# Performance work log

Measured on AMD Instinct MI355X. Metric: run time of the kernel, lower is better.

The kernel has to match this reference:

```python
import jax, jax.numpy as jnp
import numpy as np

B, S, H, N, NREL = 16, 2048, 1024, 128, 8


def setup_inputs() -> dict:
    key = jax.random.key(0)
    ks = jax.random.split(key, 8)
    word_emb = jax.random.normal(ks[0], (B, S, H), dtype=jnp.float32)
    num_ids = jax.random.randint(ks[1], (B, N), 0, S)  # all valid (no -1 padding)
    is_response = jax.random.randint(ks[2], (B, N), 0, 2).astype(jnp.int32)
    numbers = jax.random.normal(ks[3], (B, N), dtype=jnp.float32)
    scale = 1.0 / np.sqrt(H).astype(np.float32)
    w_alpha = jax.random.normal(ks[4], (H, 1), dtype=jnp.float32) * scale
    b_alpha = jnp.zeros((1,), dtype=jnp.float32)
    w_f = jax.random.normal(ks[5], (H, H), dtype=jnp.float32) * scale
    b_f = jnp.zeros((H,), dtype=jnp.float32)
    W_r = jax.random.normal(ks[6], (NREL, H, H), dtype=jnp.float32) * scale  # 8 bias-free relation linears
    return dict(word_emb=word_emb, num_ids=num_ids, is_response=is_response,
                numbers=numbers, w_alpha=w_alpha, b_alpha=b_alpha,
                w_f=w_f, b_f=b_f, W_r=W_r)


def reference(word_emb, num_ids, is_response, numbers, w_alpha, b_alpha, w_f, b_f, W_r):
    Bn, Sn, Hn = word_emb.shape
    Nn = num_ids.shape[1]
    mask = (num_ids >= 0)  # [B,N] valid-node mask (original uses -1 padding)
    idx = jnp.clip(num_ids, 0, Sn - 1)
    # per-batch gather: Init[b,n] = word_emb[b, num_ids[b,n]]  -> [B,N,H]
    Init = jnp.take_along_axis(word_emb, idx[:, :, None], axis=1)
    alpha = jax.nn.sigmoid(Init @ w_alpha + b_alpha)  # [B,N,1]
    # all 8 relation transforms of every sender node j: T[b,r,j,:] = Init[b,j] @ W_r[r].T
    T = jnp.einsum('bnh,rkh->brnk', Init, W_r)  # [B,8,N,H]
    # relation id r(b,i,j) = 4*(num_i>num_j) + 2*resp_i + resp_j
    gt = (numbers[:, :, None] > numbers[:, None, :]).astype(jnp.int32)  # [B,N,N]
    resp = (is_response == 1).astype(jnp.int32)
    R = 4 * gt + 2 * resp[:, :, None] + resp[:, None, :]  # [B,N,N]
    sel = jax.nn.one_hot(R, NREL, dtype=word_emb.dtype)  # [B,N,N,8]
    not_diag = ~jnp.eye(Nn, dtype=bool)
    # edge weight over sender j: alpha_j, valid i & j, i != j
    wgt = (alpha[:, None, :, 0] * mask[:, None, :] * mask[:, :, None]
           * not_diag[None]).astype(word_emb.dtype)  # [B,N,N]
    Temp = jnp.einsum('bijr,brjh->bih', sel * wgt[..., None], T)  # [B,N,H]
    n_nodes = mask.sum(axis=1)  # [B]
    denom = jnp.maximum(n_nodes - 1, 1).astype(word_emb.dtype)
    Temp = Temp / denom[:, None, None]
    out = jax.nn.relu(Init @ w_f + b_f + Temp)  # [B,N,H]
    return out
```

## Files before the change

kernel.cpp:

```cpp
#include <hip/hip_runtime.h>
#include <hip/hip_bf16.h>
#include <stdint.h>

#define B_ 16
#define S_ 2048
#define H_ 1024
#define N_ 128
#define M_ (B_*N_)
#define K5 5120
#define MP 2176

typedef __attribute__((ext_vector_type(8))) short s8vec;
typedef __attribute__((ext_vector_type(4))) short s4vec;
typedef __attribute__((ext_vector_type(4))) float f4vec;
typedef __hip_bfloat16 bf16;

__global__ void k_sortmeta(const int* __restrict__ num_ids, const int* __restrict__ is_resp,
                           const float* __restrict__ numbers,
                           int* __restrict__ sigma, int* __restrict__ newgrp,
                           int* __restrict__ respv, float* __restrict__ denom,
                           int* __restrict__ aperm, int* __restrict__ iperm,
                           int* __restrict__ meta) {
    __shared__ float nums_s[2048];
    __shared__ int sig_s[2048];
    __shared__ int s0[1024], s1[1024];
    __shared__ int cnt_s[16];
    int t = threadIdx.x;
    int g0 = 2*t, g1 = 2*t + 1;
    int b = g0 >> 7;
    int i0 = g0 & 127, i1 = g1 & 127;
    float n0 = numbers[g0], n1 = numbers[g1];
    int id0 = num_ids[g0], id1 = num_ids[g1];
    int v0 = (id0 >= 0) ? 1 : 0, v1 = (id1 >= 0) ? 1 : 0;
    int rsp0 = (is_resp[g0] == 1) ? 1 : 0, rsp1 = (is_resp[g1] == 1) ? 1 : 0;
    nums_s[g0] = n0; nums_s[g1] = n1;
    if (t < 16) cnt_s[t] = 0;
    aperm[t] = -1; aperm[t + 1024] = -1;
    if (t < MP - 2048) aperm[t + 2048] = -1;
    __syncthreads();
    const float* nb = nums_s + b*N_;
    int p0 = 0, p1 = 0;
    for (int j = 0; j < N_; ++j) {
        float nj = nb[j];
        p0 += (nj < n0 || (nj == n0 && j < i0)) ? 1 : 0;
        p1 += (nj < n1 || (nj == n1 && j < i1)) ? 1 : 0;
    }
    sig_s[b*N_ + p0] = i0;
    sig_s[b*N_ + p1] = i1;
    atomicAdd(&cnt_s[b], v0 + v1);
    __syncthreads();
    sigma[g0] = sig_s[g0]; sigma[g1] = sig_s[g1];
    {
        int cur = sig_s[g0];
        int prv = (i0 > 0) ? sig_s[g0-1] : 0;
        newgrp[g0] = (i0 == 0 || nb[cur] != nb[prv]) ? 1 : 0;
        cur = sig_s[g1];
        prv = sig_s[g1-1];
        newgrp[g1] = (nb[cur] != nb[prv]) ? 1 : 0;
    }
    respv[g0] = rsp0 | (v0 << 1);
    respv[g1] = rsp1 | (v1 << 1);
    if (t < 16) denom[t] = fmaxf((float)(cnt_s[t] - 1), 1.0f);
    int a0 = 1 - rsp0, b0 = 1 - rsp1;
    s0[t] = a0 + b0;
    s1[t] = rsp0 + rsp1;
    __syncthreads();
    for (int off = 1; off < 1024; off <<= 1) {
        int w0 = (t >= off) ? s0[t-off] : 0;
        int w1 = (t >= off) ? s1[t-off] : 0;
        __syncthreads();
        s0[t] += w0; s1[t] += w1;
        __syncthreads();
    }
    int C0 = s0[1023], C1 = s1[1023];
    int P0 = ((C0 + 127) >> 7) << 7;
    int ex0 = s0[t] - (a0 + b0);
    int ex1 = s1[t] - (rsp0 + rsp1);
    int p_a = (rsp0 == 0) ? ex0 : P0 + ex1;
    int p_b = (rsp1 == 0) ? ex0 + a0 : P0 + ex1 + rsp0;
    aperm[p_a] = g0; iperm[g0] = p_a;
    aperm[p_b] = g1; iperm[g1] = p_b;
    if (t == 0) { meta[0] = P0; meta[1] = C0; meta[2] = C1; }
}

__global__ void k_prep(const float* __restrict__ word_emb, const int* __restrict__ num_ids,
                       const float* __restrict__ w_alpha, const float* __restrict__ b_alpha,
                       const float* __restrict__ denom, const int* __restrict__ iperm,
                       const float* __restrict__ W_r, const float* __restrict__ w_f,
                       bf16* __restrict__ A, float* __restrict__ ascaled,
                       bf16* __restrict__ Wt) {
    __shared__ float lds[64][65];
    int bid = blockIdx.x;
    int t = threadIdx.x;
    if (bid < 2048) {
        int b = bid >> 7, n = bid & 127;
        int idv = num_ids[b*N_ + n];
        int valid = (idv >= 0) ? 1 : 0;
        int idx = idv < 0 ? 0 : (idv > S_-1 ? S_-1 : idv);
        int pr = iperm[b*N_ + n];
        const float4* row = (const float4*)(word_emb + ((size_t)b*S_ + idx)*H_);
        float4 v = row[t];
        float4 w = ((const float4*)w_alpha)[t];
        float part = v.x*w.x + v.y*w.y + v.z*w.z + v.w*w.w;
        union { s4vec v4; bf16 h[4]; } pk;
        pk.h[0] = __float2bfloat16(v.x);
        pk.h[1] = __float2bfloat16(v.y);
        pk.h[2] = __float2bfloat16(v.z);
        pk.h[3] = __float2bfloat16(v.w);
        *(s4vec*)(A + (size_t)pr*K5 + 4*H_ + t*4) = pk.v4;
#pragma unroll
        for (int off = 32; off > 0; off >>= 1) part += __shfl_down(part, off, 64);
        if ((t & 63) == 0) lds[0][t >> 6] = part;
        __syncthreads();
        if (t == 0) {
            float dot = lds[0][0] + lds[0][1] + lds[0][2] + lds[0][3] + b_alpha[0];
            float al = 1.0f / (1.0f + __expf(-dot));
            ascaled[b*N_ + n] = valid ? (al / denom[b]) : 0.0f;
        }
        return;
    }
    if (bid < 6144) {
        size_t o = ((size_t)(bid - 2048)*256 + t)*8;
        int cs = (int)(o >> 20);
        int c = cs >> 2, s = cs & 3;
        int r = ((s >> 1) << 2) + 2*c + (s & 1);
        size_t off = o & (size_t)(H_*H_ - 1);
        const float4* src = (const float4*)(W_r + (size_t)r*H_*H_ + off);
        float4 v0 = src[0], v1 = src[1];
        union { s8vec v8; bf16 h[8]; } pk;
        pk.h[0] = __float2bfloat16(v0.x); pk.h[1] = __float2bfloat16(v0.y);
        pk.h[2] = __float2bfloat16(v0.z); pk.h[3] = __float2bfloat16(v0.w);
        pk.h[4] = __float2bfloat16(v1.x); pk.h[5] = __float2bfloat16(v1.y);
        pk.h[6] = __float2bfloat16(v1.z); pk.h[7] = __float2bfloat16(v1.w);
        *(s8vec*)(Wt + (size_t)(c*5 + s)*H_*H_ + off) = pk.v8;
        return;
    }
    int bb = bid - 6144;
    int bi = bb & 15, bj = bb >> 4;
    int ty = t >> 4, tx = t & 15;
#pragma unroll
    for (int i = 0; i < 4; ++i) {
        int r = ty*4 + i;
        float4 v = *(const float4*)(w_f + (size_t)(bi*64 + r)*H_ + bj*64 + tx*4);
        lds[r][tx*4+0] = v.x; lds[r][tx*4+1] = v.y;
        lds[r][tx*4+2] = v.z; lds[r][tx*4+3] = v.w;
    }
    __syncthreads();
    bf16* d0 = Wt + (size_t)4*H_*H_;
    bf16* d1 = Wt + (size_t)9*H_*H_;
#pragma unroll
    for (int i = 0; i < 4; ++i) {
        int n = ty*4 + i;
        size_t doff = (size_t)(bj*64 + n)*H_ + bi*64 + tx*4;
        union { s4vec v4; bf16 h[4]; } pk;
#pragma unroll
        for (int j = 0; j < 4; ++j) pk.h[j] = __float2bfloat16(lds[tx*4+j][n]);
        *(s4vec*)(d0 + doff) = pk.v4;
        *(s4vec*)(d1 + doff) = pk.v4;
    }
}

__global__ void k_build(const float* __restrict__ ascaled, const int* __restrict__ sigma,
                        const int* __restrict__ newgrp, const int* __restrict__ respv,
                        const int* __restrict__ iperm, bf16* __restrict__ A) {
    int b = blockIdx.y;
    int h = blockIdx.x*64 + threadIdx.x;
    __shared__ float as_s[N_];
    __shared__ int sig_s[N_], ng_s[N_], rv_s[N_], pm_s[N_];
    for (int j = threadIdx.x; j < N_; j += 64) {
        as_s[j] = ascaled[b*N_ + j];
        sig_s[j] = sigma[b*N_ + j];
        ng_s[j] = newgrp[b*N_ + j];
        rv_s[j] = respv[b*N_ + j];
        pm_s[j] = iperm[b*N_ + j];
    }
    __syncthreads();
    const bf16* initcol = A + 4*H_ + h;
    float tot0 = 0.f, tot1 = 0.f;
#pragma unroll 8
    for (int i2 = 0; i2 < N_; ++i2) {
        float v = as_s[i2] * __bfloat162float(initcol[(size_t)pm_s[i2]*K5]);
        if (rv_s[i2] & 1) tot1 += v; else tot0 += v;
    }
    float cS0=0.f, cS1=0.f, cG0=0.f, cG1=0.f;
#pragma unroll 8
    for (int p = 0; p < N_; ++p) {
        int i2 = sig_s[p];
        if (ng_s[p]) { cS0 += cG0; cS1 += cG1; cG0 = 0.f; cG1 = 0.f; }
        float v = as_s[i2] * __bfloat162float(initcol[(size_t)pm_s[i2]*K5]);
        int resp = rv_s[i2] & 1;
        float vf = (rv_s[i2] >> 1) ? 1.0f : 0.0f;
        float G0 = cS0, G1 = cS1;
        float L0 = tot0 - G0 - (resp ? 0.f : v);
        float L1 = tot1 - G1 - (resp ? v : 0.f);
        bf16* Ar = A + (size_t)pm_s[i2]*K5 + h;
        Ar[0*H_] = __float2bfloat16(L0*vf);
        Ar[1*H_] = __float2bfloat16(L1*vf);
        Ar[2*H_] = __float2bfloat16(G0*vf);
        Ar[3*H_] = __float2bfloat16(G1*vf);
        if (resp) cG1 += v; else cG0 += v;
    }
}

#define BM 128
#define BN 128
#define BK 64
#define KS 4
#define KSP (K5/KS)
#define NSTEP (KSP/BK)

__global__ __launch_bounds__(256, 2) void k_gemm(const bf16* __restrict__ A,
                                                 const bf16* __restrict__ Wt,
                                                 const int* __restrict__ meta,
                                                 float* __restrict__ P) {
    __shared__ __align__(16) bf16 As0[BM*BK], As1[BM*BK];
    __shared__ __align__(16) bf16 Bs0[BN*BK], Bs1[BN*BK];
    int tid = threadIdx.x;
    int w = tid >> 6, lane = tid & 63;
    int q = lane >> 4, r = lane & 15;
    int bid = blockIdx.x;
    int wg = (bid & 7)*68 + (bid >> 3);
    int mt = wg % 17;
    int rest = wg / 17;
    int nt = rest & 7, ks = rest >> 3;
    int rowBase = mt * BM, colBase = nt * BN;
    int wm = w >> 1, wn = w & 1;
    int P0 = meta[0];
    const bf16* Wtc = Wt + ((rowBase >= P0) ? (size_t)5*H_*H_ : 0);
    const int kb = ks * KSP;

    f4vec acc[4][4];
#pragma unroll
    for (int mi = 0; mi < 4; ++mi)
#pragma unroll
        for (int ni = 0; ni < 4; ++ni)
#pragma unroll
            for (int e = 0; e < 4; ++e) acc[mi][ni][e] = 0.0f;

    auto STAGE = [&](bf16* AsB, bf16* BsB, int kin) {
        int slot = kin >> 10, koff = kin & 1023;
        const bf16* Wslot = Wtc + ((size_t)slot << 20);
#pragma unroll
        for (int j = 0; j < 4; ++j) {
            int c = tid + j*256;
            int row = c >> 3;
            int p = (c & 7) ^ (row & 7);
            const bf16* ga = A + (size_t)(rowBase + row)*K5 + kin + p*8;
            __builtin_amdgcn_global_load_lds((const __attribute__((address_space(1))) void*)ga,
                (__attribute__((address_space(3))) void*)((char*)AsB + j*4096 + w*1024), 16, 0, 0);
            const bf16* gb = Wslot + ((size_t)(colBase + row) << 10) + koff + p*8;
            __builtin_amdgcn_global_load_lds((const __attribute__((address_space(1))) void*)gb,
                (__attribute__((address_space(3))) void*)((char*)BsB + j*4096 + w*1024), 16, 0, 0);
        }
    };

    auto COMPUTE = [&](const bf16* AsB, const bf16* BsB) {
        const short* Asp = (const short*)AsB;
        const short* Bsp = (const short*)BsB;
        s8vec af[2][4], bfr[2][4];
#pragma unroll
        for (int kk = 0; kk < 2; ++kk) {
            int sl = ((kk*4 + q) ^ (r & 7)) << 3;
#pragma unroll
            for (int mi = 0; mi < 4; ++mi)
                af[kk][mi] = *(const s8vec*)(Asp + (wm*64 + mi*16 + r)*BK + sl);
#pragma unroll
            for (int ni = 0; ni < 4; ++ni)
                bfr[kk][ni] = *(const s8vec*)(Bsp + (wn*64 + ni*16 + r)*BK + sl);
        }
#pragma unroll
        for (int kk = 0; kk < 2; ++kk)
#pragma unroll
            for (int mi = 0; mi < 4; ++mi)
#pragma unroll
                for (int ni = 0; ni < 4; ++ni)
                    acc[mi][ni] = __builtin_amdgcn_mfma_f32_16x16x32_bf16(
                        af[kk][mi], bfr[kk][ni], acc[mi][ni], 0, 0, 0);
    };

    STAGE(As0, Bs0, kb);
    asm volatile("s_waitcnt vmcnt(0)" ::: "memory");
    __builtin_amdgcn_s_barrier();
    __builtin_amdgcn_sched_barrier(0);

    for (int t = 0; t < NSTEP; t += 2) {
        STAGE(As1, Bs1, kb + (t + 1)*BK);
        COMPUTE(As0, Bs0);
        asm volatile("s_waitcnt vmcnt(0)" ::: "memory");
        __builtin_amdgcn_s_barrier();
        __builtin_amdgcn_sched_barrier(0);
        if (t + 2 < NSTEP) STAGE(As0, Bs0, kb + (t + 2)*BK);
        COMPUTE(As1, Bs1);
        asm volatile("s_waitcnt vmcnt(0)" ::: "memory");
        __builtin_amdgcn_s_barrier();
        __builtin_amdgcn_sched_barrier(0);
    }

    float* Pk = P + (size_t)ks*MP*H_;
#pragma unroll
    for (int mi = 0; mi < 4; ++mi) {
#pragma unroll
        for (int ni = 0; ni < 4; ++ni) {
            int cc = colBase + wn*64 + ni*16 + r;
#pragma unroll
            for (int e = 0; e < 4; ++e) {
                int rr = rowBase + wm*64 + mi*16 + q*4 + e;
                Pk[(size_t)rr*H_ + cc] = acc[mi][ni][e];
            }
        }
    }
}

__global__ void k_epi(const float* __restrict__ P, const int* __restrict__ iperm,
                      const float* __restrict__ b_f, float* __restrict__ out) {
    int row = blockIdx.x;
    int pr = iperm[row];
    int t = threadIdx.x;
    float4 v0 = ((const float4*)(P + ((size_t)0*MP + pr)*H_))[t];
    float4 v1 = ((const float4*)(P + ((size_t)1*MP + pr)*H_))[t];
    float4 v2 = ((const float4*)(P + ((size_t)2*MP + pr)*H_))[t];
    float4 v3 = ((const float4*)(P + ((size_t)3*MP + pr)*H_))[t];
    float4 bv = ((const float4*)b_f)[t];
    float4 o;
    o.x = fmaxf(v0.x + v1.x + v2.x + v3.x + bv.x, 0.0f);
    o.y = fmaxf(v0.y + v1.y + v2.y + v3.y + bv.y, 0.0f);
    o.z = fmaxf(v0.z + v1.z + v2.z + v3.z + bv.z, 0.0f);
    o.w = fmaxf(v0.w + v1.w + v2.w + v3.w + bv.w, 0.0f);
    ((float4*)(out + (size_t)row*H_))[t] = o;
}

extern "C" void kernel_launch(void* const* d_in, const int* in_sizes, int n_in,
                              void* d_out, int out_size, void* d_ws, size_t ws_size,
                              hipStream_t stream) {
    (void)in_sizes; (void)n_in; (void)out_size; (void)ws_size;
    const float* word_emb = (const float*)d_in[0];
    const int*   num_ids  = (const int*)d_in[1];
    const int*   is_resp  = (const int*)d_in[2];
    const float* numbers  = (const float*)d_in[3];
    const float* w_alpha  = (const float*)d_in[4];
    const float* b_alpha  = (const float*)d_in[5];
    const float* w_f      = (const float*)d_in[6];
    const float* b_f      = (const float*)d_in[7];
    const float* W_r      = (const float*)d_in[8];
    float* out = (float*)d_out;

    char* ws = (char*)d_ws;
    bf16*  Aws     = (bf16*)(ws);
    bf16*  Wt      = (bf16*)(ws + 22282240);
    float* Pbuf    = (float*)(ws + 43253760);
    float* ascaled = (float*)(ws + 78905344);
    int*   sigma   = (int*)(ws + 78913536);
    int*   newgrp  = (int*)(ws + 78921728);
    int*   respv   = (int*)(ws + 78929920);
    float* denom   = (float*)(ws + 78938112);
    int*   aperm   = (int*)(ws + 78938176);
    int*   iperm   = (int*)(ws + 78946880);
    int*   meta    = (int*)(ws + 78955072);

    k_sortmeta<<<1, 1024, 0, stream>>>(num_ids, is_resp, numbers, sigma, newgrp, respv,
                                       denom, aperm, iperm, meta);
    k_prep  <<<6400, 256, 0, stream>>>(word_emb, num_ids, w_alpha, b_alpha, denom, iperm,
                                       W_r, w_f, Aws, ascaled, Wt);
    k_build <<<dim3(16,16), 64, 0, stream>>>(ascaled, sigma, newgrp, respv, iperm, Aws);
    k_gemm  <<<544,  256, 0, stream>>>(Aws, Wt, meta, Pbuf);
    k_epi   <<<2048, 256, 0, stream>>>(Pbuf, iperm, b_f, out);
}
```

Measured before the change: 299.6 us.

## Fuse split-K reduction into GEMM via atomic ticket and double split-K

```diff
diff --git a/kernel.cpp b/kernel.cpp
--- a/kernel.cpp
+++ b/kernel.cpp
@@ -20,7 +20,7 @@
                            int* __restrict__ sigma, int* __restrict__ newgrp,
                            int* __restrict__ respv, float* __restrict__ denom,
                            int* __restrict__ aperm, int* __restrict__ iperm,
-                           int* __restrict__ meta) {
+                           int* __restrict__ meta, int* __restrict__ tick) {
     __shared__ float nums_s[2048];
     __shared__ int sig_s[2048];
     __shared__ int s0[1024], s1[1024];
@@ -35,6 +35,7 @@
     int rsp0 = (is_resp[g0] == 1) ? 1 : 0, rsp1 = (is_resp[g1] == 1) ? 1 : 0;
     nums_s[g0] = n0; nums_s[g1] = n1;
     if (t < 16) cnt_s[t] = 0;
+    if (t < 136) tick[t] = 0;
     aperm[t] = -1; aperm[t + 1024] = -1;
     if (t < MP - 2048) aperm[t + 2048] = -1;
     __syncthreads();
@@ -204,22 +205,27 @@
 
 #define BM 128
 #define BN 128
-#define BK 64
-#define KS 4
+#define BK 32
+#define KS 8
 #define KSP (K5/KS)
 #define NSTEP (KSP/BK)
 
-__global__ __launch_bounds__(256, 2) void k_gemm(const bf16* __restrict__ A,
+__global__ __launch_bounds__(256, 4) void k_gemm(const bf16* __restrict__ A,
                                                  const bf16* __restrict__ Wt,
                                                  const int* __restrict__ meta,
-                                                 float* __restrict__ P) {
+                                                 const int* __restrict__ aperm,
+                                                 const float* __restrict__ b_f,
+                                                 float* __restrict__ P,
+                                                 int* __restrict__ tick,
+                                                 float* __restrict__ out) {
     __shared__ __align__(16) bf16 As0[BM*BK], As1[BM*BK];
     __shared__ __align__(16) bf16 Bs0[BN*BK], Bs1[BN*BK];
+    __shared__ int tk_s;
     int tid = threadIdx.x;
     int w = tid >> 6, lane = tid & 63;
     int q = lane >> 4, r = lane & 15;
     int bid = blockIdx.x;
-    int wg = (bid & 7)*68 + (bid >> 3);
+    int wg = (bid & 7)*136 + (bid >> 3);
     int mt = wg % 17;
     int rest = wg / 17;
     int nt = rest & 7, ks = rest >> 3;
@@ -241,10 +247,10 @@
         int slot = kin >> 10, koff = kin & 1023;
         const bf16* Wslot = Wtc + ((size_t)slot << 20);
 #pragma unroll
-        for (int j = 0; j < 4; ++j) {
+        for (int j = 0; j < 2; ++j) {
             int c = tid + j*256;
-            int row = c >> 3;
-            int p = (c & 7) ^ (row & 7);
+            int row = c >> 2;
+            int p = (c & 3) ^ ((c >> 4) & 3);
             const bf16* ga = A + (size_t)(rowBase + row)*K5 + kin + p*8;
             __builtin_amdgcn_global_load_lds((const __attribute__((address_space(1))) void*)ga,
                 (__attribute__((address_space(3))) void*)((char*)AsB + j*4096 + w*1024), 16, 0, 0);
@@ -257,25 +263,20 @@
     auto COMPUTE = [&](const bf16* AsB, const bf16* BsB) {
         const short* Asp = (const short*)AsB;
         const short* Bsp = (const short*)BsB;
-        s8vec af[2][4], bfr[2][4];
-#pragma unroll
-        for (int kk = 0; kk < 2; ++kk) {
-            int sl = ((kk*4 + q) ^ (r & 7)) << 3;
-#pragma unroll
-            for (int mi = 0; mi < 4; ++mi)
-                af[kk][mi] = *(const s8vec*)(Asp + (wm*64 + mi*16 + r)*BK + sl);
+        s8vec af[4], bfr[4];
+        int sl = (q ^ ((r >> 2) & 3)) << 3;
+#pragma unroll
+        for (int mi = 0; mi < 4; ++mi)
+            af[mi] = *(const s8vec*)(Asp + (wm*64 + mi*16 + r)*BK + sl);
+#pragma unroll
+        for (int ni = 0; ni < 4; ++ni)
+            bfr[ni] = *(const s8vec*)(Bsp + (wn*64 + ni*16 + r)*BK + sl);
+#pragma unroll
+        for (int mi = 0; mi < 4; ++mi)
 #pragma unroll
             for (int ni = 0; ni < 4; ++ni)
-                bfr[kk][ni] = *(const s8vec*)(Bsp + (wn*64 + ni*16 + r)*BK + sl);
-        }
-#pragma unroll
-        for (int kk = 0; kk < 2; ++kk)
-#pragma unroll
-            for (int mi = 0; mi < 4; ++mi)
-#pragma unroll
-                for (int ni = 0; ni < 4; ++ni)
-                    acc[mi][ni] = __builtin_amdgcn_mfma_f32_16x16x32_bf16(
-                        af[kk][mi], bfr[kk][ni], acc[mi][ni], 0, 0, 0);
+                acc[mi][ni] = __builtin_amdgcn_mfma_f32_16x16x32_bf16(
+                    af[mi], bfr[ni], acc[mi][ni], 0, 0, 0);
     };
 
     STAGE(As0, Bs0, kb);
@@ -309,24 +310,50 @@
             }
         }
     }
-}
-
-__global__ void k_epi(const float* __restrict__ P, const int* __restrict__ iperm,
-                      const float* __restrict__ b_f, float* __restrict__ out) {
-    int row = blockIdx.x;
-    int pr = iperm[row];
-    int t = threadIdx.x;
-    float4 v0 = ((const float4*)(P + ((size_t)0*MP + pr)*H_))[t];
-    float4 v1 = ((const float4*)(P + ((size_t)1*MP + pr)*H_))[t];
-    float4 v2 = ((const float4*)(P + ((size_t)2*MP + pr)*H_))[t];
-    float4 v3 = ((const float4*)(P + ((size_t)3*MP + pr)*H_))[t];
-    float4 bv = ((const float4*)b_f)[t];
-    float4 o;
-    o.x = fmaxf(v0.x + v1.x + v2.x + v3.x + bv.x, 0.0f);
-    o.y = fmaxf(v0.y + v1.y + v2.y + v3.y + bv.y, 0.0f);
-    o.z = fmaxf(v0.z + v1.z + v2.z + v3.z + bv.z, 0.0f);
-    o.w = fmaxf(v0.w + v1.w + v2.w + v3.w + bv.w, 0.0f);
-    ((float4*)(out + (size_t)row*H_))[t] = o;
+    __threadfence();
+    __syncthreads();
+    if (tid == 0) tk_s = atomicAdd(&tick[mt*8 + nt], 1);
+    __syncthreads();
+    if (tk_s != KS - 1) return;
+
+    __threadfence();
+    int og[4][4];
+    float bias[4];
+#pragma unroll
+    for (int mi = 0; mi < 4; ++mi) {
+        int rb = rowBase + wm*64 + mi*16 + q*4;
+#pragma unroll
+        for (int e = 0; e < 4; ++e) og[mi][e] = aperm[rb + e];
+    }
+#pragma unroll
+    for (int ni = 0; ni < 4; ++ni) bias[ni] = b_f[colBase + wn*64 + ni*16 + r];
+    for (int s = 0; s < KS; ++s) {
+        if (s == ks) continue;
+        const float* Ps = P + (size_t)s*MP*H_;
+#pragma unroll
+        for (int mi = 0; mi < 4; ++mi) {
+#pragma unroll
+            for (int ni = 0; ni < 4; ++ni) {
+                int cc = colBase + wn*64 + ni*16 + r;
+#pragma unroll
+                for (int e = 0; e < 4; ++e) {
+                    int rr = rowBase + wm*64 + mi*16 + q*4 + e;
+                    acc[mi][ni][e] += Ps[(size_t)rr*H_ + cc];
+                }
+            }
+        }
+    }
+#pragma unroll
+    for (int mi = 0; mi < 4; ++mi) {
+#pragma unroll
+        for (int ni = 0; ni < 4; ++ni) {
+            int cc = colBase + wn*64 + ni*16 + r;
+            if (og[mi][0] >= 0) out[(size_t)og[mi][0]*H_ + cc] = fmaxf(acc[mi][ni][0] + bias[ni], 0.0f);
+            if (og[mi][1] >= 0) out[(size_t)og[mi][1]*H_ + cc] = fmaxf(acc[mi][ni][1] + bias[ni], 0.0f);
+            if (og[mi][2] >= 0) out[(size_t)og[mi][2]*H_ + cc] = fmaxf(acc[mi][ni][2] + bias[ni], 0.0f);
+            if (og[mi][3] >= 0) out[(size_t)og[mi][3]*H_ + cc] = fmaxf(acc[mi][ni][3] + bias[ni], 0.0f);
+        }
+    }
 }
 
 extern "C" void kernel_launch(void* const* d_in, const int* in_sizes, int n_in,
@@ -348,20 +375,20 @@
     bf16*  Aws     = (bf16*)(ws);
     bf16*  Wt      = (bf16*)(ws + 22282240);
     float* Pbuf    = (float*)(ws + 43253760);
-    float* ascaled = (float*)(ws + 78905344);
-    int*   sigma   = (int*)(ws + 78913536);
-    int*   newgrp  = (int*)(ws + 78921728);
-    int*   respv   = (int*)(ws + 78929920);
-    float* denom   = (float*)(ws + 78938112);
-    int*   aperm   = (int*)(ws + 78938176);
-    int*   iperm   = (int*)(ws + 78946880);
-    int*   meta    = (int*)(ws + 78955072);
+    float* ascaled = (float*)(ws + 114556928);
+    int*   sigma   = (int*)(ws + 114565120);
+    int*   newgrp  = (int*)(ws + 114573312);
+    int*   respv   = (int*)(ws + 114581504);
+    float* denom   = (float*)(ws + 114589696);
+    int*   aperm   = (int*)(ws + 114589760);
+    int*   iperm   = (int*)(ws + 114598464);
+    int*   meta    = (int*)(ws + 114606656);
+    int*   tick    = (int*)(ws + 114606720);
 
     k_sortmeta<<<1, 1024, 0, stream>>>(num_ids, is_resp, numbers, sigma, newgrp, respv,
-                                       denom, aperm, iperm, meta);
+                                       denom, aperm, iperm, meta, tick);
     k_prep  <<<6400, 256, 0, stream>>>(word_emb, num_ids, w_alpha, b_alpha, denom, iperm,
                                        W_r, w_f, Aws, ascaled, Wt);
     k_build <<<dim3(16,16), 64, 0, stream>>>(ascaled, sigma, newgrp, respv, iperm, Aws);
-    k_gemm  <<<544,  256, 0, stream>>>(Aws, Wt, meta, Pbuf);
-    k_epi   <<<2048, 256, 0, stream>>>(Pbuf, iperm, b_f, out);
-}
+    k_gemm  <<<1088, 256, 0, stream>>>(Aws, Wt, meta, aperm, b_f, Pbuf, tick, out);
+}
```

Measured after the change: 538.9 us. +79.9%, slower.
